# Performance work log

Measured on AMD Instinct MI355X. Metric: run time of the kernel, lower is better.

Reference implementation:

```python
import jax, jax.numpy as jnp
from jax import lax
import numpy as np

H = 32  # hidden size
IN = 3  # input dim
NCLASS = 7
T = 30  # sequence length used by forward (indexes t=29)


def _lstm_layer(x, W_ih, W_hh, b_ih, b_hh):
    """One unidirectional LSTM layer, batch_first x: [B,T,D] -> [B,T,H].
    PyTorch gate order: i, f, g, o."""
    B = x.shape[0]
    # Precompute input contribution for all timesteps: [B,T,4H]
    xg = jnp.einsum('btd,gd->btg', x, W_ih) + b_ih + b_hh

    def step(carry, xg_t):
        h, c = carry
        gates = xg_t + h @ W_hh.T  # [B,4H]
        i, f, g, o = jnp.split(gates, 4, axis=-1)
        i = jax.nn.sigmoid(i)
        f = jax.nn.sigmoid(f)
        g = jnp.tanh(g)
        o = jax.nn.sigmoid(o)
        c = f * c + i * g
        h = o * jnp.tanh(c)
        return (h, c), h

    h0 = jnp.zeros((B, H), x.dtype)
    (_, _), hs = lax.scan(step, (h0, h0), jnp.swapaxes(xg, 0, 1))  # hs: [T,B,H]
    return jnp.swapaxes(hs, 0, 1)


def setup_inputs() -> dict:
    key = jax.random.key(0)
    ks = jax.random.split(key, 20)
    B = 65536
    s = 1.0 / np.sqrt(H)  # PyTorch LSTM/Linear init scale
    u = lambda k, shape: jax.random.uniform(k, shape, jnp.float32, -s, s)
    inp = {'X': jax.random.normal(ks[0], (B, T, IN), jnp.float32)}
    dims_in = [IN, H, H]
    for l in range(3):
        inp[f'W_ih{l}'] = u(ks[1 + 4 * l], (4 * H, dims_in[l]))
        inp[f'W_hh{l}'] = u(ks[2 + 4 * l], (4 * H, H))
        inp[f'b_ih{l}'] = u(ks[3 + 4 * l], (4 * H,))
        inp[f'b_hh{l}'] = u(ks[4 + 4 * l], (4 * H,))
    inp['W1'] = u(ks[13], (H // 2, H))
    inp['b1'] = u(ks[14], (H // 2,))
    inp['W2'] = u(ks[15], (NCLASS, H // 2))
    inp['b2'] = u(ks[16], (NCLASS,))
    return inp


def reference(X, W_ih0, W_hh0, b_ih0, b_hh0, W_ih1, W_hh1, b_ih1, b_hh1,
              W_ih2, W_hh2, b_ih2, b_hh2, W1, b1, W2, b2):
    h = _lstm_layer(X, W_ih0, W_hh0, b_ih0, b_hh0)
    h = _lstm_layer(h, W_ih1, W_hh1, b_ih1, b_hh1)
    h = _lstm_layer(h, W_ih2, W_hh2, b_ih2, b_hh2)
    last = h[:, T - 1, :]  # [B,H]
    out = last @ W1.T + b1
    out = out @ W2.T + b2  # [B,7]; Softmax is defined but not applied in forward
    return out
```

## Files before the change

kernel.cpp:

```cpp
#include <hip/hip_runtime.h>
#include <stdint.h>

#define T_STEPS 30
#define HDIM 32
#define BTOT 65536

typedef __bf16 bf16_t;
typedef bf16_t bf16x8 __attribute__((ext_vector_type(8)));
typedef float f32x4 __attribute__((ext_vector_type(4)));

__device__ __forceinline__ float fast_sigmoid(float x) {
    return __builtin_amdgcn_rcpf(1.0f + __expf(-x));
}
__device__ __forceinline__ float fast_tanh(float x) {
    return 2.0f * __builtin_amdgcn_rcpf(1.0f + __expf(-2.0f * x)) - 1.0f;
}

template <int LI, bool SAVE>
__device__ __forceinline__ void cell(
    int lane, int lrow, int kgrp,
    const bf16_t* __restrict__ wb,
    const float (&breg)[3][8],
    bf16x8 ain,
    bf16x8& ah,
    float (&cst)[3][2][4],
    float (&hsave)[2][4],
    bf16_t (*hb)[32])
{
    constexpr int WIH_OFF = ((LI == 0) ? 0 : (LI == 1) ? 2 : 4) * 4096;
    constexpr int WHH_OFF = WIH_OFF + 4096;

    f32x4 acc[8];
#pragma unroll
    for (int tl = 0; tl < 8; ++tl) {
        const float bb = breg[LI][tl];
        acc[tl][0] = bb; acc[tl][1] = bb; acc[tl][2] = bb; acc[tl][3] = bb;
    }
#pragma unroll
    for (int tl = 0; tl < 8; ++tl) {
        bf16x8 bfr = *(const bf16x8*)(wb + WIH_OFF + (tl << 9) + (lane << 3));
        acc[tl] = __builtin_amdgcn_mfma_f32_16x16x32_bf16(ain, bfr, acc[tl], 0, 0, 0);
    }
#pragma unroll
    for (int tl = 0; tl < 8; ++tl) {
        bf16x8 bfr = *(const bf16x8*)(wb + WHH_OFF + (tl << 9) + (lane << 3));
        acc[tl] = __builtin_amdgcn_mfma_f32_16x16x32_bf16(ah, bfr, acc[tl], 0, 0, 0);
    }
#pragma unroll
    for (int mt = 0; mt < 2; ++mt) {
#pragma unroll
        for (int r = 0; r < 4; ++r) {
            const float iv = fast_sigmoid(acc[0 + mt][r]);
            const float fv = fast_sigmoid(acc[2 + mt][r]);
            const float gv = fast_tanh(acc[4 + mt][r]);
            const float ov = fast_sigmoid(acc[6 + mt][r]);
            const float cc = fv * cst[LI][mt][r] + iv * gv;
            cst[LI][mt][r] = cc;
            const float hv = ov * fast_tanh(cc);
            if (SAVE) hsave[mt][r] = hv;
            hb[kgrp * 4 + r][mt * 16 + lrow] = (bf16_t)hv;
        }
    }
    ah = *(const bf16x8*)(&hb[lrow][kgrp << 3]);
}

__global__ __launch_bounds__(256, 2) void lstm3_fused(
    const float* __restrict__ X,
    const float* __restrict__ Wih0, const float* __restrict__ Whh0,
    const float* __restrict__ bih0, const float* __restrict__ bhh0,
    const float* __restrict__ Wih1, const float* __restrict__ Whh1,
    const float* __restrict__ bih1, const float* __restrict__ bhh1,
    const float* __restrict__ Wih2, const float* __restrict__ Whh2,
    const float* __restrict__ bih2, const float* __restrict__ bhh2,
    const float* __restrict__ W1, const float* __restrict__ b1,
    const float* __restrict__ W2, const float* __restrict__ b2,
    float* __restrict__ out)
{
    __shared__ alignas(16) bf16_t wfrag[6 * 4096];
    __shared__ float bias_s[3][128];
    __shared__ alignas(16) bf16_t hbuf[4][16][32];
    __shared__ alignas(16) float hfin[4][16][32];

    const int tid = threadIdx.x;

    auto stage = [&](int mat, const float* __restrict__ w, int K) {
        for (int p = tid; p < 4096; p += 256) {
            const int tile = p >> 9;
            const int r = p & 511;
            const int ln = r >> 3;
            const int j = r & 7;
            const int k = ((ln >> 4) << 3) + j;
            const int n = (tile << 4) + (ln & 15);
            const float v = (k < K) ? w[n * K + k] : 0.0f;
            wfrag[mat * 4096 + p] = (bf16_t)v;
        }
    };
    stage(0, Wih0, 3);
    stage(1, Whh0, HDIM);
    stage(2, Wih1, HDIM);
    stage(3, Whh1, HDIM);
    stage(4, Wih2, HDIM);
    stage(5, Whh2, HDIM);
    for (int p = tid; p < 384; p += 256) {
        const int l = p >> 7, n = p & 127;
        float v;
        if (l == 0)      v = bih0[n] + bhh0[n];
        else if (l == 1) v = bih1[n] + bhh1[n];
        else             v = bih2[n] + bhh2[n];
        bias_s[l][n] = v;
    }
    __syncthreads();

    const int wave = tid >> 6;
    const int lane = tid & 63;
    const int lrow = lane & 15;
    const int kgrp = lane >> 4;
    const int b0 = blockIdx.x * 64 + wave * 16;

    float breg[3][8];
#pragma unroll
    for (int l = 0; l < 3; ++l)
#pragma unroll
        for (int tl = 0; tl < 8; ++tl)
            breg[l][tl] = bias_s[l][tl * 16 + lrow];

    float cst[3][2][4];
#pragma unroll
    for (int l = 0; l < 3; ++l)
#pragma unroll
        for (int mt = 0; mt < 2; ++mt)
#pragma unroll
            for (int r = 0; r < 4; ++r) cst[l][mt][r] = 0.0f;

    bf16x8 ah0, ah1, ah2;
#pragma unroll
    for (int j = 0; j < 8; ++j) { ah0[j] = (bf16_t)0.0f; ah1[j] = (bf16_t)0.0f; ah2[j] = (bf16_t)0.0f; }
    float h2keep[2][4];
#pragma unroll
    for (int mt = 0; mt < 2; ++mt)
#pragma unroll
        for (int r = 0; r < 4; ++r) h2keep[mt][r] = 0.0f;

    bf16_t (*hb)[32] = hbuf[wave];

    const float* xlane = X + (size_t)(b0 + lrow) * (T_STEPS * 3);
    float cx0 = xlane[0], cx1 = xlane[1], cx2 = xlane[2];

    for (int t = 0; t < T_STEPS; ++t) {
        const int tn = (t < T_STEPS - 1) ? (t + 1) : (T_STEPS - 1);
        const float nx0 = xlane[tn * 3 + 0];
        const float nx1 = xlane[tn * 3 + 1];
        const float nx2 = xlane[tn * 3 + 2];

        unsigned lz = 0;
        asm volatile("" : "+v"(lz));
        const bf16_t* wbt = wfrag + lz;

        bf16x8 ax;
#pragma unroll
        for (int j = 0; j < 8; ++j) ax[j] = (bf16_t)0.0f;
        if (kgrp == 0) { ax[0] = (bf16_t)cx0; ax[1] = (bf16_t)cx1; ax[2] = (bf16_t)cx2; }

        cell<0, false>(lane, lrow, kgrp, wbt, breg, ax,  ah0, cst, h2keep, hb);
        cell<1, false>(lane, lrow, kgrp, wbt, breg, ah0, ah1, cst, h2keep, hb);
        cell<2, true >(lane, lrow, kgrp, wbt, breg, ah1, ah2, cst, h2keep, hb);

        cx0 = nx0; cx1 = nx1; cx2 = nx2;
    }

#pragma unroll
    for (int mt = 0; mt < 2; ++mt)
#pragma unroll
        for (int r = 0; r < 4; ++r)
            hfin[wave][kgrp * 4 + r][mt * 16 + lrow] = h2keep[mt][r];

    if (lane < 16) {
        float hv[HDIM];
#pragma unroll
        for (int k = 0; k < HDIM; ++k) hv[k] = hfin[wave][lane][k];
        float y1[16];
#pragma unroll
        for (int o = 0; o < 16; ++o) {
            float a = b1[o];
#pragma unroll
            for (int k = 0; k < HDIM; ++k) a += hv[k] * W1[o * 32 + k];
            y1[o] = a;
        }
        const int b = b0 + lane;
#pragma unroll
        for (int q = 0; q < 7; ++q) {
            float a = b2[q];
#pragma unroll
            for (int o = 0; o < 16; ++o) a += y1[o] * W2[q * 16 + o];
            out[b * 7 + q] = a;
        }
    }
}

extern "C" void kernel_launch(void* const* d_in, const int* in_sizes, int n_in,
                              void* d_out, int out_size, void* d_ws, size_t ws_size,
                              hipStream_t stream) {
    (void)in_sizes; (void)n_in; (void)d_ws; (void)ws_size; (void)out_size;
    const float* X    = (const float*)d_in[0];
    const float* Wih0 = (const float*)d_in[1];
    const float* Whh0 = (const float*)d_in[2];
    const float* bih0 = (const float*)d_in[3];
    const float* bhh0 = (const float*)d_in[4];
    const float* Wih1 = (const float*)d_in[5];
    const float* Whh1 = (const float*)d_in[6];
    const float* bih1 = (const float*)d_in[7];
    const float* bhh1 = (const float*)d_in[8];
    const float* Wih2 = (const float*)d_in[9];
    const float* Whh2 = (const float*)d_in[10];
    const float* bih2 = (const float*)d_in[11];
    const float* bhh2 = (const float*)d_in[12];
    const float* W1   = (const float*)d_in[13];
    const float* b1   = (const float*)d_in[14];
    const float* W2   = (const float*)d_in[15];
    const float* b2   = (const float*)d_in[16];
    float* out = (float*)d_out;

    dim3 grid(BTOT / 64), block(256);
    hipLaunchKernelGGL(lstm3_fused, grid, block, 0, stream,
                       X, Wih0, Whh0, bih0, bhh0, Wih1, Whh1, bih1, bhh1,
                       Wih2, Whh2, bih2, bhh2, W1, b1, W2, b2, out);
}
```

Before: 348.1 us.

## Pipeline LSTM layers across waves with register-resident weights and exp2 gates

Each block now handles 16 sequences with three waves, one per LSTM layer. The layers run as a wavefront pipeline, with wave l at timestep s-l, passing hidden states through double-buffered shared memory and a __syncthreads per step. Weights are held as bf16 MFMA fragments in registers rather than shared memory, and biases are folded into an exp2-based sigmoid/tanh with log2e prescaling. This shortens the serial dependency chain per wave and drops repeated LDS weight loads, at the cost of block-wide barriers every step, 4x more blocks, and higher register pressure.

```diff
diff --git a/kernel.cpp b/kernel.cpp
--- a/kernel.cpp
+++ b/kernel.cpp
@@ -2,69 +2,25 @@
 #include <stdint.h>
 
 #define T_STEPS 30
-#define HDIM 32
 #define BTOT 65536
+#define L2E 1.4426950408889634f
 
 typedef __bf16 bf16_t;
 typedef bf16_t bf16x8 __attribute__((ext_vector_type(8)));
 typedef float f32x4 __attribute__((ext_vector_type(4)));
 
-__device__ __forceinline__ float fast_sigmoid(float x) {
-    return __builtin_amdgcn_rcpf(1.0f + __expf(-x));
-}
-__device__ __forceinline__ float fast_tanh(float x) {
-    return 2.0f * __builtin_amdgcn_rcpf(1.0f + __expf(-2.0f * x)) - 1.0f;
-}
-
-template <int LI, bool SAVE>
-__device__ __forceinline__ void cell(
-    int lane, int lrow, int kgrp,
-    const bf16_t* __restrict__ wb,
-    const float (&breg)[3][8],
-    bf16x8 ain,
-    bf16x8& ah,
-    float (&cst)[3][2][4],
-    float (&hsave)[2][4],
-    bf16_t (*hb)[32])
-{
-    constexpr int WIH_OFF = ((LI == 0) ? 0 : (LI == 1) ? 2 : 4) * 4096;
-    constexpr int WHH_OFF = WIH_OFF + 4096;
-
-    f32x4 acc[8];
-#pragma unroll
-    for (int tl = 0; tl < 8; ++tl) {
-        const float bb = breg[LI][tl];
-        acc[tl][0] = bb; acc[tl][1] = bb; acc[tl][2] = bb; acc[tl][3] = bb;
-    }
-#pragma unroll
-    for (int tl = 0; tl < 8; ++tl) {
-        bf16x8 bfr = *(const bf16x8*)(wb + WIH_OFF + (tl << 9) + (lane << 3));
-        acc[tl] = __builtin_amdgcn_mfma_f32_16x16x32_bf16(ain, bfr, acc[tl], 0, 0, 0);
-    }
-#pragma unroll
-    for (int tl = 0; tl < 8; ++tl) {
-        bf16x8 bfr = *(const bf16x8*)(wb + WHH_OFF + (tl << 9) + (lane << 3));
-        acc[tl] = __builtin_amdgcn_mfma_f32_16x16x32_bf16(ah, bfr, acc[tl], 0, 0, 0);
-    }
-#pragma unroll
-    for (int mt = 0; mt < 2; ++mt) {
-#pragma unroll
-        for (int r = 0; r < 4; ++r) {
-            const float iv = fast_sigmoid(acc[0 + mt][r]);
-            const float fv = fast_sigmoid(acc[2 + mt][r]);
-            const float gv = fast_tanh(acc[4 + mt][r]);
-            const float ov = fast_sigmoid(acc[6 + mt][r]);
-            const float cc = fv * cst[LI][mt][r] + iv * gv;
-            cst[LI][mt][r] = cc;
-            const float hv = ov * fast_tanh(cc);
-            if (SAVE) hsave[mt][r] = hv;
-            hb[kgrp * 4 + r][mt * 16 + lrow] = (bf16_t)hv;
-        }
-    }
-    ah = *(const bf16x8*)(&hb[lrow][kgrp << 3]);
-}
-
-__global__ __launch_bounds__(256, 2) void lstm3_fused(
+__device__ __forceinline__ float exp2_fast(float x) {
+#if __has_builtin(__builtin_amdgcn_exp2f)
+    return __builtin_amdgcn_exp2f(x);
+#else
+    return __expf(x * 0.6931471805599453f);
+#endif
+}
+__device__ __forceinline__ float rcp_fast(float x) {
+    return __builtin_amdgcn_rcpf(x);
+}
+
+__global__ __launch_bounds__(192, 3) void lstm3_pipe(
     const float* __restrict__ X,
     const float* __restrict__ Wih0, const float* __restrict__ Whh0,
     const float* __restrict__ bih0, const float* __restrict__ bhh0,
@@ -76,123 +32,147 @@
     const float* __restrict__ W2, const float* __restrict__ b2,
     float* __restrict__ out)
 {
-    __shared__ alignas(16) bf16_t wfrag[6 * 4096];
-    __shared__ float bias_s[3][128];
-    __shared__ alignas(16) bf16_t hbuf[4][16][32];
-    __shared__ alignas(16) float hfin[4][16][32];
-
-    const int tid = threadIdx.x;
-
-    auto stage = [&](int mat, const float* __restrict__ w, int K) {
-        for (int p = tid; p < 4096; p += 256) {
-            const int tile = p >> 9;
-            const int r = p & 511;
-            const int ln = r >> 3;
-            const int j = r & 7;
-            const int k = ((ln >> 4) << 3) + j;
-            const int n = (tile << 4) + (ln & 15);
-            const float v = (k < K) ? w[n * K + k] : 0.0f;
-            wfrag[mat * 4096 + p] = (bf16_t)v;
-        }
-    };
-    stage(0, Wih0, 3);
-    stage(1, Whh0, HDIM);
-    stage(2, Wih1, HDIM);
-    stage(3, Whh1, HDIM);
-    stage(4, Wih2, HDIM);
-    stage(5, Whh2, HDIM);
-    for (int p = tid; p < 384; p += 256) {
-        const int l = p >> 7, n = p & 127;
-        float v;
-        if (l == 0)      v = bih0[n] + bhh0[n];
-        else if (l == 1) v = bih1[n] + bhh1[n];
-        else             v = bih2[n] + bhh2[n];
-        bias_s[l][n] = v;
-    }
-    __syncthreads();
-
+    __shared__ alignas(16) bf16_t xch[5 * 640];
+    __shared__ float hfin[16][33];
+
+    const int tid  = threadIdx.x;
     const int wave = tid >> 6;
     const int lane = tid & 63;
     const int lrow = lane & 15;
     const int kgrp = lane >> 4;
-    const int b0 = blockIdx.x * 64 + wave * 16;
-
-    float breg[3][8];
-#pragma unroll
-    for (int l = 0; l < 3; ++l)
-#pragma unroll
-        for (int tl = 0; tl < 8; ++tl)
-            breg[l][tl] = bias_s[l][tl * 16 + lrow];
-
-    float cst[3][2][4];
-#pragma unroll
-    for (int l = 0; l < 3; ++l)
+    const int b0   = blockIdx.x * 16;
+
+    const float* Wih; const float* Whh; const float* bihp; const float* bhhp; int K;
+    if (wave == 0)      { Wih = Wih0; Whh = Whh0; bihp = bih0; bhhp = bhh0; K = 3;  }
+    else if (wave == 1) { Wih = Wih1; Whh = Whh1; bihp = bih1; bhhp = bhh1; K = 32; }
+    else                { Wih = Wih2; Whh = Whh2; bihp = bih2; bhhp = bhh2; K = 32; }
+
+    bf16x8 wih[8], whh[8];
+    float bs[8];
+#pragma unroll
+    for (int tl = 0; tl < 8; ++tl) {
+        const int n = tl * 16 + lrow;
+        bf16x8 fi, fh;
+        if (K == 32) {
+            const float* p = Wih + n * 32 + kgrp * 8;
+#pragma unroll
+            for (int j = 0; j < 8; ++j) fi[j] = (bf16_t)p[j];
+        } else {
+#pragma unroll
+            for (int j = 0; j < 8; ++j) {
+                const int k = kgrp * 8 + j;
+                fi[j] = (k < 3) ? (bf16_t)Wih[n * 3 + k] : (bf16_t)(0.0f);
+            }
+        }
+        const float* q = Whh + n * 32 + kgrp * 8;
+#pragma unroll
+        for (int j = 0; j < 8; ++j) fh[j] = (bf16_t)q[j];
+        wih[tl] = fi;
+        whh[tl] = fh;
+        const float b = bihp[n] + bhhp[n];
+        bs[tl] = b * (((tl >> 1) == 2) ? (-2.0f * L2E) : (-L2E));
+    }
+
+    float cst[2][4];
+    float h2keep[2][4];
+#pragma unroll
+    for (int mt = 0; mt < 2; ++mt)
+#pragma unroll
+        for (int r = 0; r < 4; ++r) { cst[mt][r] = 0.0f; h2keep[mt][r] = 0.0f; }
+
+    bf16x8 ah;
+#pragma unroll
+    for (int j = 0; j < 8; ++j) ah[j] = (bf16_t)(0.0f);
+
+    const float* xlane = X + (size_t)(b0 + lrow) * (T_STEPS * 3);
+    float cx0 = 0.0f, cx1 = 0.0f, cx2 = 0.0f;
+    if (wave == 0) { cx0 = xlane[0]; cx1 = xlane[1]; cx2 = xlane[2]; }
+
+    const int wslot = (wave == 0) ? 0 : 2;
+    const int rslot = (wave == 1) ? 0 : 2;
+
+    for (int s = 0; s < T_STEPS + 2; ++s) {
+        const int tw = s - wave;
+        if (tw >= 0 && tw < T_STEPS) {
+            const int par = tw & 1;
+            bf16x8 ain;
+            if (wave == 0) {
+                const int tn = (tw < T_STEPS - 1) ? tw + 1 : T_STEPS - 1;
+                const float nx0 = xlane[tn * 3 + 0];
+                const float nx1 = xlane[tn * 3 + 1];
+                const float nx2 = xlane[tn * 3 + 2];
+#pragma unroll
+                for (int j = 0; j < 8; ++j) ain[j] = (bf16_t)(0.0f);
+                if (kgrp == 0) {
+                    ain[0] = (bf16_t)cx0; ain[1] = (bf16_t)cx1; ain[2] = (bf16_t)cx2;
+                }
+                cx0 = nx0; cx1 = nx1; cx2 = nx2;
+            } else {
+                ain = *(const bf16x8*)(xch + (rslot + par) * 640 + lrow * 40 + (kgrp << 3));
+            }
+
+            f32x4 acc[8];
+#pragma unroll
+            for (int tl = 0; tl < 8; ++tl) {
+                f32x4 z; z[0] = 0.0f; z[1] = 0.0f; z[2] = 0.0f; z[3] = 0.0f;
+                acc[tl] = __builtin_amdgcn_mfma_f32_16x16x32_bf16(ain, wih[tl], z, 0, 0, 0);
+            }
+#pragma unroll
+            for (int tl = 0; tl < 8; ++tl)
+                acc[tl] = __builtin_amdgcn_mfma_f32_16x16x32_bf16(ah, whh[tl], acc[tl], 0, 0, 0);
+
+            bf16_t* wb = xch + (((wave == 2) ? 4 : (wslot + par)) * 640);
+            const bool sv = (wave == 2) && (tw == T_STEPS - 1);
+#pragma unroll
+            for (int mt = 0; mt < 2; ++mt) {
+#pragma unroll
+                for (int r = 0; r < 4; ++r) {
+                    const float iv = rcp_fast(1.0f + exp2_fast(acc[0 + mt][r] * (-L2E) + bs[0 + mt]));
+                    const float fv = rcp_fast(1.0f + exp2_fast(acc[2 + mt][r] * (-L2E) + bs[2 + mt]));
+                    const float ge = exp2_fast(acc[4 + mt][r] * (-2.0f * L2E) + bs[4 + mt]);
+                    const float gv = 2.0f * rcp_fast(1.0f + ge) - 1.0f;
+                    const float ov = rcp_fast(1.0f + exp2_fast(acc[6 + mt][r] * (-L2E) + bs[6 + mt]));
+                    const float cc = fv * cst[mt][r] + iv * gv;
+                    cst[mt][r] = cc;
+                    const float te = exp2_fast(cc * (-2.0f * L2E));
+                    const float th = 2.0f * rcp_fast(1.0f + te) - 1.0f;
+                    const float hv = ov * th;
+                    if (sv) h2keep[mt][r] = hv;
+                    wb[(kgrp * 4 + r) * 40 + mt * 16 + lrow] = (bf16_t)hv;
+                }
+            }
+            ah = *(const bf16x8*)(wb + lrow * 40 + (kgrp << 3));
+        }
+        __syncthreads();
+    }
+
+    if (wave == 2) {
 #pragma unroll
         for (int mt = 0; mt < 2; ++mt)
 #pragma unroll
-            for (int r = 0; r < 4; ++r) cst[l][mt][r] = 0.0f;
-
-    bf16x8 ah0, ah1, ah2;
-#pragma unroll
-    for (int j = 0; j < 8; ++j) { ah0[j] = (bf16_t)0.0f; ah1[j] = (bf16_t)0.0f; ah2[j] = (bf16_t)0.0f; }
-    float h2keep[2][4];
-#pragma unroll
-    for (int mt = 0; mt < 2; ++mt)
-#pragma unroll
-        for (int r = 0; r < 4; ++r) h2keep[mt][r] = 0.0f;
-
-    bf16_t (*hb)[32] = hbuf[wave];
-
-    const float* xlane = X + (size_t)(b0 + lrow) * (T_STEPS * 3);
-    float cx0 = xlane[0], cx1 = xlane[1], cx2 = xlane[2];
-
-    for (int t = 0; t < T_STEPS; ++t) {
-        const int tn = (t < T_STEPS - 1) ? (t + 1) : (T_STEPS - 1);
-        const float nx0 = xlane[tn * 3 + 0];
-        const float nx1 = xlane[tn * 3 + 1];
-        const float nx2 = xlane[tn * 3 + 2];
-
-        unsigned lz = 0;
-        asm volatile("" : "+v"(lz));
-        const bf16_t* wbt = wfrag + lz;
-
-        bf16x8 ax;
-#pragma unroll
-        for (int j = 0; j < 8; ++j) ax[j] = (bf16_t)0.0f;
-        if (kgrp == 0) { ax[0] = (bf16_t)cx0; ax[1] = (bf16_t)cx1; ax[2] = (bf16_t)cx2; }
-
-        cell<0, false>(lane, lrow, kgrp, wbt, breg, ax,  ah0, cst, h2keep, hb);
-        cell<1, false>(lane, lrow, kgrp, wbt, breg, ah0, ah1, cst, h2keep, hb);
-        cell<2, true >(lane, lrow, kgrp, wbt, breg, ah1, ah2, cst, h2keep, hb);
-
-        cx0 = nx0; cx1 = nx1; cx2 = nx2;
-    }
-
-#pragma unroll
-    for (int mt = 0; mt < 2; ++mt)
-#pragma unroll
-        for (int r = 0; r < 4; ++r)
-            hfin[wave][kgrp * 4 + r][mt * 16 + lrow] = h2keep[mt][r];
-
-    if (lane < 16) {
-        float hv[HDIM];
-#pragma unroll
-        for (int k = 0; k < HDIM; ++k) hv[k] = hfin[wave][lane][k];
-        float y1[16];
-#pragma unroll
-        for (int o = 0; o < 16; ++o) {
-            float a = b1[o];
-#pragma unroll
-            for (int k = 0; k < HDIM; ++k) a += hv[k] * W1[o * 32 + k];
-            y1[o] = a;
-        }
-        const int b = b0 + lane;
-#pragma unroll
-        for (int q = 0; q < 7; ++q) {
-            float a = b2[q];
-#pragma unroll
-            for (int o = 0; o < 16; ++o) a += y1[o] * W2[q * 16 + o];
-            out[b * 7 + q] = a;
+            for (int r = 0; r < 4; ++r)
+                hfin[kgrp * 4 + r][mt * 16 + lrow] = h2keep[mt][r];
+
+        if (lane < 16) {
+            float hv[32];
+#pragma unroll
+            for (int k = 0; k < 32; ++k) hv[k] = hfin[lane][k];
+            float y1[16];
+#pragma unroll
+            for (int o = 0; o < 16; ++o) {
+                float a = b1[o];
+#pragma unroll
+                for (int k = 0; k < 32; ++k) a += hv[k] * W1[o * 32 + k];
+                y1[o] = a;
+            }
+            const int b = b0 + lane;
+#pragma unroll
+            for (int q = 0; q < 7; ++q) {
+                float a = b2[q];
+#pragma unroll
+                for (int o = 0; o < 16; ++o) a += y1[o] * W2[q * 16 + o];
+                out[b * 7 + q] = a;
+            }
         }
     }
 }
@@ -220,8 +200,8 @@
     const float* b2   = (const float*)d_in[16];
     float* out = (float*)d_out;
 
-    dim3 grid(BTOT / 64), block(256);
-    hipLaunchKernelGGL(lstm3_fused, grid, block, 0, stream,
+    dim3 grid(BTOT / 16), block(192);
+    hipLaunchKernelGGL(lstm3_pipe, grid, block, 0, stream,
                        X, Wih0, Whh0, bih0, bhh0, Wih1, Whh1, bih1, bhh1,
                        Wih2, Whh2, bih2, bhh2, W1, b1, W2, b2, out);
 }
```

Result: slower. 391.3 us (+12.4%).
